# Optimization experiments

Hardware: AMD Instinct MI355X
Metric: run time of the kernel (lower is better)

Reference implementation:

```python
import jax, jax.numpy as jnp
import numpy as np

T_LATENCY = 2  # refractory latency (timesteps), from init_kwargs
FS_SCALE = 10.0  # FastSigmoid surrogate scale


@jax.custom_vjp
def fast_sigmoid_spike(u):
    return (u > 0).astype(u.dtype)

def _fs_fwd(u):
    return fast_sigmoid_spike(u), u

def _fs_bwd(u, g):
    return (g / (FS_SCALE * jnp.abs(u) + 1.0) ** 2,)

fast_sigmoid_spike.defvjp(_fs_fwd, _fs_bwd)


def setup_inputs() -> dict:
    key = jax.random.key(0)
    k1, k2, k3, k4 = jax.random.split(key, 4)
    B, N, T = 64, 1024, 512
    x = jax.random.normal(k1, (B, N, T), dtype=jnp.float32)
    beta = jax.random.uniform(k2, (N,), jnp.float32, 0.3, 0.95)   # leak
    p = jax.random.uniform(k3, (N,), jnp.float32, 0.5, 0.95)      # adaptation decay
    b = jax.random.uniform(k4, (N,), jnp.float32, 0.5, 1.5)       # adaptation strength
    return {"x": x, "beta": beta, "p": p, "b": b}


def reference(x, beta, p, b):
    # clamped effective params (matches torch @property accessors)
    beta_c = jnp.clip(beta, 0.001, 0.999)
    p_c = jnp.clip(jnp.abs(p), 0.0, 0.999)
    b_c = jnp.clip(jnp.abs(b), 0.001, 1.0)

    B, N, T = x.shape
    xt = jnp.moveaxis(x, 2, 0)  # [T, B, N]

    def step(carry, x_t):
        mem, spikes, refac, a, v_th = carry
        # spike-triggered refractory reset, then mask input during refractory window
        refac = jnp.where(spikes > 0, 0.0, refac)
        ic = jnp.where(refac < T_LATENCY, 0.0, x_t)
        refac = refac + 1.0
        # leaky integration
        new_mem = mem * beta_c + ic
        s = fast_sigmoid_spike(new_mem - v_th)
        # reset-by-subtraction-to-zero with detached spikes (detach_spike_grad=True)
        mem = new_mem * (1.0 - jax.lax.stop_gradient(s))
        # adaptive threshold
        a = p_c * a + s
        v_th = 1.0 + b_c * a
        return (mem, s, refac, a, v_th), s

    z = jnp.zeros((B, N), x.dtype)
    init = (z, z, jnp.full((B, N), float(T_LATENCY), x.dtype), z,
            jnp.ones((B, N), x.dtype))
    _, spikes_seq = jax.lax.scan(step, init, xt)  # [T, B, N]
    return jnp.moveaxis(spikes_seq, 0, 2)  # [B, N, T]
```

## Files before the change

### kernel.cpp

```cpp
#include <hip/hip_runtime.h>

#pragma clang fp contract(off)

#define ROWS    64
#define T_LEN   512
#define CHUNK   64
#define NCHUNK  (T_LEN / CHUNK)
#define NV      16
#define BUFW    (ROWS * CHUNK)
#define NPARAM  1024

typedef float f4_nt __attribute__((ext_vector_type(4)));

#define BARRIER() asm volatile("s_waitcnt lgkmcnt(0)\n\ts_barrier" ::: "memory")

#define GLOAD16(gp, lp)                                                \
    __builtin_amdgcn_global_load_lds(                                  \
        (const __attribute__((address_space(1))) void*)(gp),           \
        (__attribute__((address_space(3))) void*)(lp), 16, 0, 0)

__global__ __launch_bounds__(192) void snn_fwd(
    const float* __restrict__ x,
    const float* __restrict__ beta,
    const float* __restrict__ p,
    const float* __restrict__ bparam,
    float* __restrict__ out)
{
    __shared__ __align__(16) float inbuf[3][BUFW];
    __shared__ __align__(16) unsigned int outw[ROWS][4];

    const int tid     = threadIdx.x;
    const int wid     = tid >> 6;
    const int lane    = tid & 63;
    const int rowBase = blockIdx.x * ROWS;

    const float4* __restrict__ xv = (const float4*)x;
    float4* __restrict__ ov       = (float4*)out;

    const int t16 = lane & 15;
    const int r4  = lane >> 4;
    const int gEven = (rowBase + r4) * (T_LEN / 4) + (t16 ^ r4);
    const int gOdd  = gEven ^ 4;
    const int gq = (rowBase + r4) * (T_LEN / 4) + t16;

    float mem = 0.0f, refac = 2.0f, a = 0.0f, vth = 1.0f, ps = 0.0f;
    float beta_c = 0.f, p_c = 0.f, b_c = 0.f;
    const int swl   = (lane & 3) | (((lane >> 2) & 1) << 2);
    const int cbase = lane * NV;

    if (wid == 0) {
        const int n = (rowBase + lane) & (NPARAM - 1);
        beta_c = fminf(fmaxf(beta[n], 0.001f), 0.999f);
        p_c    = fminf(fabsf(p[n]), 0.999f);
        b_c    = fminf(fmaxf(fabsf(bparam[n]), 0.001f), 1.0f);
    }

    unsigned int b0 = 0, b1 = 0;

    auto step = [&](float xt, unsigned int msk, unsigned int& bw) {
        refac = (ps > 0.0f) ? 0.0f : refac;
        const float ic = (refac < 2.0f) ? 0.0f : xt;
        refac += 1.0f;
        const float nm   = __fadd_rn(__fmul_rn(mem, beta_c), ic);
        const float diff = __fsub_rn(nm, vth);
        const bool  sp   = diff > 0.0f;
        const float s    = sp ? 1.0f : 0.0f;
        bw |= sp ? msk : 0u;
        mem = sp ? 0.0f : nm;
        a   = __fadd_rn(__fmul_rn(p_c, a), s);
        vth = __fadd_rn(1.0f, __fmul_rn(b_c, a));
        ps  = s;
    };

    auto issue = [&](int c, int buf) {
        float* lb = &inbuf[buf][0];
        #pragma unroll
        for (int it = 0; it < NV; ++it) {
            const int gidx = ((it & 1) ? gOdd : gEven)
                           + it * 4 * (T_LEN / 4) + c * NV;
            GLOAD16(&xv[gidx], lb + it * 256);
        }
    };

    auto drain = [&](int c) {
        #pragma unroll
        for (int it = 0; it < NV; ++it) {
            const int row = r4 + 4 * it;
            const uint2 bits = *(const uint2*)&outw[row][0];
            const unsigned int w = (t16 & 8) ? bits.y : bits.x;
            const int sh = (t16 & 7) * 4;
            float4 sv;
            sv.x = (float)((w >> (sh + 0)) & 1u);
            sv.y = (float)((w >> (sh + 1)) & 1u);
            sv.z = (float)((w >> (sh + 2)) & 1u);
            sv.w = (float)((w >> (sh + 3)) & 1u);
            __builtin_nontemporal_store(
                *reinterpret_cast<f4_nt*>(&sv),
                reinterpret_cast<f4_nt*>(&ov[gq + c * NV + it * 4 * (T_LEN / 4)]));
        }
    };

    if (wid == 1) {
        issue(0, 0);
        issue(1, 1);
        asm volatile("s_waitcnt vmcnt(16)" ::: "memory");
    }
    BARRIER();

    int km3 = 0;
    #pragma unroll 1
    for (int k = 0; k < NCHUNK; ++k) {
        if (wid == 0) {
            b0 = 0; b1 = 0;
            const float4* ib = (const float4*)inbuf[km3];
            #pragma unroll
            for (int g = 0; g < NV; ++g) {
                const float4 v = ib[cbase + (g ^ swl)];
                const int t = 4 * g;
                if (t < 32) {
                    step(v.x, 1u << (t + 0), b0);
                    step(v.y, 1u << (t + 1), b0);
                    step(v.z, 1u << (t + 2), b0);
                    step(v.w, 1u << (t + 3), b0);
                } else {
                    step(v.x, 1u << (t - 32), b1);
                    step(v.y, 1u << (t - 31), b1);
                    step(v.z, 1u << (t - 30), b1);
                    step(v.w, 1u << (t - 29), b1);
                }
            }
        } else if (wid == 1) {
            if (k + 2 < NCHUNK) {
                int nb = km3 + 2; if (nb >= 3) nb -= 3;
                issue(k + 2, nb);
            }
        } else {
            if (k > 0) drain(k - 1);
        }
        BARRIER();
        if (wid == 0) {
            *(uint2*)&outw[lane][0] = make_uint2(b0, b1);
        } else if (wid == 1) {
            if (k < NCHUNK - 2)
                asm volatile("s_waitcnt vmcnt(16)" ::: "memory");
            else if (k == NCHUNK - 2)
                asm volatile("s_waitcnt vmcnt(0)" ::: "memory");
        }
        BARRIER();
        ++km3; if (km3 == 3) km3 = 0;
    }
    if (wid == 2) drain(NCHUNK - 1);
}

extern "C" void kernel_launch(void* const* d_in, const int* in_sizes, int n_in,
                              void* d_out, int out_size, void* d_ws, size_t ws_size,
                              hipStream_t stream) {
    const float* x    = (const float*)d_in[0];
    const float* beta = (const float*)d_in[1];
    const float* p    = (const float*)d_in[2];
    const float* b    = (const float*)d_in[3];
    float* out        = (float*)d_out;

    const int BN = 64 * 1024;
    snn_fwd<<<dim3(BN / ROWS), dim3(192), 0, stream>>>(x, beta, p, b, out);
}
```

Measured before the change: 250.5 us.

## Drop drain wave; buffer all spike bits in LDS and store after loop

Removes the third wavefront that streamed each chunk's spike bits to global memory during the scan. The compute wave now keeps all 512 bits per row in a 64x16-word LDS array, and after the scan both waves expand the bits to floats and write the whole output tile with nontemporal stores. Each loop iteration needs only one barrier instead of two, and blocks shrink to 128 threads, so more blocks can fit per CU. In exchange, output stores no longer overlap with the recurrence inside a block and all happen at the end, leaving other resident blocks to hide that write traffic.

```diff
diff --git a/kernel.cpp b/kernel.cpp
--- a/kernel.cpp
+++ b/kernel.cpp
@@ -19,7 +19,7 @@
         (const __attribute__((address_space(1))) void*)(gp),           \
         (__attribute__((address_space(3))) void*)(lp), 16, 0, 0)
 
-__global__ __launch_bounds__(192) void snn_fwd(
+__global__ __launch_bounds__(128) void snn_fwd(
     const float* __restrict__ x,
     const float* __restrict__ beta,
     const float* __restrict__ p,
@@ -27,7 +27,7 @@
     float* __restrict__ out)
 {
     __shared__ __align__(16) float inbuf[3][BUFW];
-    __shared__ __align__(16) unsigned int outw[ROWS][4];
+    __shared__ __align__(16) unsigned int bitlds[ROWS][16];
 
     const int tid     = threadIdx.x;
     const int wid     = tid >> 6;
@@ -41,7 +41,6 @@
     const int r4  = lane >> 4;
     const int gEven = (rowBase + r4) * (T_LEN / 4) + (t16 ^ r4);
     const int gOdd  = gEven ^ 4;
-    const int gq = (rowBase + r4) * (T_LEN / 4) + t16;
 
     float mem = 0.0f, refac = 2.0f, a = 0.0f, vth = 1.0f, ps = 0.0f;
     float beta_c = 0.f, p_c = 0.f, b_c = 0.f;
@@ -82,24 +81,6 @@
         }
     };
 
-    auto drain = [&](int c) {
-        #pragma unroll
-        for (int it = 0; it < NV; ++it) {
-            const int row = r4 + 4 * it;
-            const uint2 bits = *(const uint2*)&outw[row][0];
-            const unsigned int w = (t16 & 8) ? bits.y : bits.x;
-            const int sh = (t16 & 7) * 4;
-            float4 sv;
-            sv.x = (float)((w >> (sh + 0)) & 1u);
-            sv.y = (float)((w >> (sh + 1)) & 1u);
-            sv.z = (float)((w >> (sh + 2)) & 1u);
-            sv.w = (float)((w >> (sh + 3)) & 1u);
-            __builtin_nontemporal_store(
-                *reinterpret_cast<f4_nt*>(&sv),
-                reinterpret_cast<f4_nt*>(&ov[gq + c * NV + it * 4 * (T_LEN / 4)]));
-        }
-    };
-
     if (wid == 1) {
         issue(0, 0);
         issue(1, 1);
@@ -129,18 +110,12 @@
                     step(v.w, 1u << (t - 29), b1);
                 }
             }
-        } else if (wid == 1) {
+            *(uint2*)&bitlds[lane][2 * k] = make_uint2(b0, b1);
+        } else {
             if (k + 2 < NCHUNK) {
                 int nb = km3 + 2; if (nb >= 3) nb -= 3;
                 issue(k + 2, nb);
             }
-        } else {
-            if (k > 0) drain(k - 1);
-        }
-        BARRIER();
-        if (wid == 0) {
-            *(uint2*)&outw[lane][0] = make_uint2(b0, b1);
-        } else if (wid == 1) {
             if (k < NCHUNK - 2)
                 asm volatile("s_waitcnt vmcnt(16)" ::: "memory");
             else if (k == NCHUNK - 2)
@@ -149,7 +124,21 @@
         BARRIER();
         ++km3; if (km3 == 3) km3 = 0;
     }
-    if (wid == 2) drain(NCHUNK - 1);
+
+    const int obase = rowBase * (T_LEN / 4);
+    #pragma unroll 4
+    for (int i = 0; i < ROWS; ++i) {
+        const unsigned int w = bitlds[i][tid >> 3];
+        const int s = (tid & 7) * 4;
+        float4 sv;
+        sv.x = (float)((w >> (s + 0)) & 1u);
+        sv.y = (float)((w >> (s + 1)) & 1u);
+        sv.z = (float)((w >> (s + 2)) & 1u);
+        sv.w = (float)((w >> (s + 3)) & 1u);
+        __builtin_nontemporal_store(
+            *reinterpret_cast<f4_nt*>(&sv),
+            reinterpret_cast<f4_nt*>(&ov[obase + i * 128 + tid]));
+    }
 }
 
 extern "C" void kernel_launch(void* const* d_in, const int* in_sizes, int n_in,
@@ -162,5 +151,5 @@
     float* out        = (float*)d_out;
 
     const int BN = 64 * 1024;
-    snn_fwd<<<dim3(BN / ROWS), dim3(192), 0, stream>>>(x, beta, p, b, out);
+    snn_fwd<<<dim3(BN / ROWS), dim3(128), 0, stream>>>(x, beta, p, b, out);
 }
```

Measured after the change: 244.9 us. 1.02x faster.
